# Kernel tuning notes

Measured on AMD Instinct MI355X. Metric: run time of the kernel, lower is better.

Reference implementation:

```python
import jax, jax.numpy as jnp
from jax import lax
import numpy as np


def make_hippo_matrix(N):
    P = np.sqrt(1 + 2 * np.arange(N))
    A = P[:, None] * P[None, :]
    A = np.tril(A) - np.diag(np.arange(N))
    return jnp.asarray(-A, dtype=jnp.float32)


def setup_inputs() -> dict:
    key = jax.random.key(0)
    k1, k2, k3, k4, k5 = jax.random.split(key, 5)
    Bsz, L, H, N = 16, 2048, 512, 64
    dt_min, dt_max = 0.001, 0.1
    u = jax.random.normal(k1, (Bsz, L, H), dtype=jnp.float32)
    B_ssm = jax.random.normal(k2, (N, 1), dtype=jnp.float32)
    C_ssm = jax.random.normal(k3, (1, N), dtype=jnp.float32)
    D_skip = jax.random.normal(k4, (1,), dtype=jnp.float32)
    log_dt = (jax.random.uniform(k5, (1,), dtype=jnp.float32)
              * (np.log(dt_max) - np.log(dt_min)) + np.log(dt_min))
    return {"u": u, "B_ssm": B_ssm, "C_ssm": C_ssm, "D_skip": D_skip, "log_dt": log_dt}


def reference(u, B_ssm, C_ssm, D_skip, log_dt):
    Bsz, L, H = u.shape
    N = B_ssm.shape[0]
    A = make_hippo_matrix(N)  # fixed HiPPO buffer (non-trainable)

    # --- discretize: A_bar = expm(dt*A); B_bar = A^{-1} (A_bar - I) B ---
    dt = jnp.exp(log_dt)  # (1,)
    A_bar = jax.scipy.linalg.expm(dt * A)  # (N, N)
    B_bar = jnp.linalg.solve(A, (A_bar - jnp.eye(N, dtype=A.dtype)) @ B_ssm)  # (N, 1)

    # --- kernel K[k] = C @ A_bar^k @ B_bar, k = 0..L-1, via scan ---
    def step(power, _):
        kk = (C_ssm @ power)[0, 0]
        return A_bar @ power, kk
    _, K = lax.scan(step, B_bar, None, length=L)  # (L,)

    # torch F.conv1d is cross-correlation; with padding L-1 and keeping the
    # first L outputs this equals a causal convolution with the FLIPPED kernel:
    #   y[t] = sum_{m=0}^{t} K[L-1-m] * u[t-m]
    Krev = K[::-1]
    n_fft = 2 * L  # linear (non-circular) convolution
    Uf = jnp.fft.rfft(u, n=n_fft, axis=1)            # (B, n_fft//2+1, H)
    Kf = jnp.fft.rfft(Krev, n=n_fft)                 # (n_fft//2+1,)
    y_conv = jnp.fft.irfft(Uf * Kf[None, :, None], n=n_fft, axis=1)[:, :L, :]
    y = y_conv.astype(u.dtype) + D_skip * u
    return y
```

## Files before the change

kernel.cpp:

```cpp
#include <hip/hip_runtime.h>
#include <math.h>


typedef short short8 __attribute__((ext_vector_type(8)));
typedef short short4v __attribute__((ext_vector_type(4)));
typedef float f32x4 __attribute__((ext_vector_type(4)));

#define SWMASK 28
__device__ __forceinline__ int swz(int r, int c) {
  return (r << 6) + (c ^ (r & SWMASK));
}
__device__ __forceinline__ float Aval(int i, int j) {
  if (i > j)  return -(float)(sqrt(2.0 * i + 1.0) * sqrt(2.0 * j + 1.0));
  if (i == j) return -(float)(i + 1);
  return 0.0f;
}
__device__ __forceinline__ unsigned rne_bf16(float x) {
  unsigned u = __float_as_uint(x);
  return (u + 0x7FFFu + ((u >> 16) & 1u)) >> 16;
}
__device__ __forceinline__ float invfact(int k) {
  switch (k) {
    case 0: return 1.0f;            case 1: return 1.0f;
    case 2: return 0.5f;            case 3: return (float)(1.0/6.0);
    case 4: return (float)(1.0/24.0);       case 5: return (float)(1.0/120.0);
    case 6: return (float)(1.0/720.0);      case 7: return (float)(1.0/5040.0);
    case 8: return (float)(1.0/40320.0);    default: return (float)(1.0/362880.0);
  }
}
__device__ __forceinline__ int slotU(int row, int kg) {
  return (row << 6) + ((kg ^ (row & 7)) << 3);
}
__device__ __forceinline__ float bf2f(unsigned short s) {
  return __uint_as_float(((unsigned)s) << 16);
}
__device__ __forceinline__ unsigned short bfh(float x) {
  return (unsigned short)rne_bf16(x);
}
__device__ __forceinline__ unsigned short bfl(float x, unsigned short h) {
  return (unsigned short)rne_bf16(x - __uint_as_float(((unsigned)h) << 16));
}

__device__ __forceinline__ void mmMFMA(
    const unsigned short* rowLh, const unsigned short* rowLl,
    const unsigned short* colRh, const unsigned short* colRl,
    unsigned short* oColH, unsigned short* oColL,
    unsigned short* oRowH, unsigned short* oRowL,
    float* oF32, const float* Xg, float cI, float cX, int tid) {
  const int lane = tid & 63, w = tid >> 6;
  const int g = lane >> 4, m = lane & 15;
  const bool doN = (oColH != nullptr) || (oF32 != nullptr);
  const bool doT = (oRowH != nullptr);
  f32x4 an[4], at[4];

  if (doN) {
    short8 ah[2], al[2];
#pragma unroll
    for (int kt = 0; kt < 2; ++kt) {
      ah[kt] = *(const short8*)&rowLh[slotU(16 * w + m, 4 * kt + g)];
      al[kt] = *(const short8*)&rowLl[slotU(16 * w + m, 4 * kt + g)];
    }
#pragma unroll
    for (int nt = 0; nt < 4; ++nt) {
      an[nt] = (f32x4){0.f, 0.f, 0.f, 0.f};
#pragma unroll
      for (int kt = 0; kt < 2; ++kt) {
        short8 bh = *(const short8*)&colRh[slotU(16 * nt + m, 4 * kt + g)];
        short8 bl = *(const short8*)&colRl[slotU(16 * nt + m, 4 * kt + g)];
        an[nt] = __builtin_amdgcn_mfma_f32_16x16x32_bf16(ah[kt], bh, an[nt], 0, 0, 0);
        an[nt] = __builtin_amdgcn_mfma_f32_16x16x32_bf16(ah[kt], bl, an[nt], 0, 0, 0);
        an[nt] = __builtin_amdgcn_mfma_f32_16x16x32_bf16(al[kt], bh, an[nt], 0, 0, 0);
      }
      if (Xg) {
#pragma unroll
        for (int r = 0; r < 4; ++r) {
          int rc = 16 * w + 4 * g + r, cc = 16 * nt + m;
          float gv = cX * Xg[(rc << 6) + (cc ^ (rc & 28))];
          if (rc == cc) gv += cI;
          an[nt][r] += gv;
        }
      }
    }
  }
  if (doT) {
    short8 ah[2], al[2];
#pragma unroll
    for (int kt = 0; kt < 2; ++kt) {
      ah[kt] = *(const short8*)&colRh[slotU(16 * w + m, 4 * kt + g)];
      al[kt] = *(const short8*)&colRl[slotU(16 * w + m, 4 * kt + g)];
    }
#pragma unroll
    for (int nt = 0; nt < 4; ++nt) {
      at[nt] = (f32x4){0.f, 0.f, 0.f, 0.f};
#pragma unroll
      for (int kt = 0; kt < 2; ++kt) {
        short8 bh = *(const short8*)&rowLh[slotU(16 * nt + m, 4 * kt + g)];
        short8 bl = *(const short8*)&rowLl[slotU(16 * nt + m, 4 * kt + g)];
        at[nt] = __builtin_amdgcn_mfma_f32_16x16x32_bf16(ah[kt], bh, at[nt], 0, 0, 0);
        at[nt] = __builtin_amdgcn_mfma_f32_16x16x32_bf16(ah[kt], bl, at[nt], 0, 0, 0);
        at[nt] = __builtin_amdgcn_mfma_f32_16x16x32_bf16(al[kt], bh, at[nt], 0, 0, 0);
      }
      if (Xg) {
        int rc = 16 * nt + m;
        int cb = 16 * w + 4 * g;
        f32x4 xv = *(const f32x4*)&Xg[(rc << 6) + (cb ^ (rc & 28))];
#pragma unroll
        for (int r = 0; r < 4; ++r) {
          float gv = cX * xv[r];
          if (rc == cb + r) gv += cI;
          at[nt][r] += gv;
        }
      }
    }
  }
  __syncthreads();
  const int k0 = 16 * w + 4 * g;
  if (doN) {
#pragma unroll
    for (int nt = 0; nt < 4; ++nt) {
      if (oColH) {
        short4v h4, l4;
#pragma unroll
        for (int r = 0; r < 4; ++r) {
          unsigned short h = bfh(an[nt][r]);
          h4[r] = (short)h;
          l4[r] = (short)bfl(an[nt][r], h);
        }
        int s = slotU(16 * nt + m, k0 >> 3) + (k0 & 7);
        *(short4v*)&oColH[s] = h4;
        *(short4v*)&oColL[s] = l4;
      }
      if (oF32) {
#pragma unroll
        for (int r = 0; r < 4; ++r) {
          int rc = k0 + r;
          oF32[(rc << 6) + ((16 * nt + m) ^ (rc & 28))] = an[nt][r];
        }
      }
    }
  }
  if (doT) {
#pragma unroll
    for (int nt = 0; nt < 4; ++nt) {
      short4v h4, l4;
#pragma unroll
      for (int r = 0; r < 4; ++r) {
        unsigned short h = bfh(at[nt][r]);
        h4[r] = (short)h;
        l4[r] = (short)bfl(at[nt][r], h);
      }
      int s = slotU(16 * nt + m, k0 >> 3) + (k0 & 7);
      *(short4v*)&oRowH[s] = h4;
      *(short4v*)&oRowL[s] = l4;
    }
  }
  __syncthreads();
}

__global__ __launch_bounds__(256) void prep_quant(
    const float* __restrict__ u, const float* __restrict__ B_ssm,
    const float* __restrict__ C_ssm, const float* __restrict__ D_skip,
    const float* __restrict__ log_dt, uint4* __restrict__ rg_hi,
    uint4* __restrict__ rg_lo, int* __restrict__ wsi,
    uint4* __restrict__ ubf) {
  __shared__ __align__(16) float smem[16384];
  const int tid = threadIdx.x;

  if (blockIdx.x != 0) {
    int q = blockIdx.x - 1;
    int b = q >> 7, rem = q & 127;
    int tc = rem >> 1, hf = rem & 1;
    int t0 = (tc << 5) + (hf << 4);
    float* S = smem;
#pragma unroll
    for (int r = 0; r < 8; ++r) {
      int s = tid + (r << 8);
      int row = s >> 7, c4 = (s & 127) << 2;
      float4 v = *(const float4*)(u + ((((b << 11) + t0 + row) << 9) + c4));
      *(float4*)&S[row * 520 + c4] = v;
    }
    __syncthreads();
#pragma unroll
    for (int r = 0; r < 4; ++r) {
      int gidx = tid + (r << 8);
      int jnG = gidx >> 5;
      int gl = (gidx >> 4) & 1;
      int hm = gidx & 15;
      int gg = (hf << 1) | gl;
      int h = (jnG << 4) + hm;
      int tb = gl << 3;
      unsigned pk[4];
#pragma unroll
      for (int q2 = 0; q2 < 4; ++q2) {
        unsigned lo = rne_bf16(S[(tb + 2 * q2) * 520 + h]);
        unsigned hi = rne_bf16(S[(tb + 2 * q2 + 1) * 520 + h]);
        pk[q2] = lo | (hi << 16);
      }
      ubf[(((b << 6) | tc) << 11) | (jnG << 6) | (gg << 4) | hm] =
          make_uint4(pk[0], pk[1], pk[2], pk[3]);
    }
    return;
  }

  float* b0 = smem;
  float* b1 = smem + 4096;
  float* b2 = smem + 8192;
  float* b3 = smem + 12288;
  unsigned short* RH = (unsigned short*)b2;
  unsigned short* RL = RH + 4096;
  unsigned short* CH = (unsigned short*)b3;
  unsigned short* CL = CH + 4096;
  unsigned short* X2H = (unsigned short*)b1;
  unsigned short* X2L = X2H + 4096;
  double* Pd = (double*)b3;
  const int lane = tid & 63, wv = tid >> 6;
  const float dtf = expf(log_dt[0]);

  if (tid < 64) {
    double p = sqrt(2.0 * tid + 1.0);
    Pd[tid] = p;
    double s = p;
#pragma unroll
    for (int off = 1; off < 64; off <<= 1) {
      double t = __shfl_down(s, off, 64);
      if (tid + off < 64) s += t;
    }
    b2[tid] = (float)((tid + 1.0) + p * (s - p));
  }
  __syncthreads();
  float maxc = 0.f;
  for (int j = 0; j < 64; ++j) maxc = fmaxf(maxc, b2[j]);
  int iE;
  frexpf(dtf * maxc, &iE);
  int sExp = iE > 0 ? iE : 0;
  const float scale = ldexpf(dtf, -sExp);
  __syncthreads();

  const int r0i = (tid & 15) << 2, c0i = (tid >> 4) << 2;
  double pr_[4], pc_[4];
#pragma unroll
  for (int i = 0; i < 4; ++i) pr_[i] = Pd[r0i + i];
#pragma unroll
  for (int j = 0; j < 4; ++j) pc_[j] = Pd[c0i + j];
  __syncthreads();
  float xv[4][4];
  unsigned short xh[4][4], xl[4][4];
#pragma unroll
  for (int i = 0; i < 4; ++i)
#pragma unroll
    for (int j = 0; j < 4; ++j) {
      int ri = r0i + i, cj = c0i + j;
      float a;
      if (ri > cj)       a = -(float)(pr_[i] * pc_[j]);
      else if (ri == cj) a = -(float)(ri + 1);
      else               a = 0.0f;
      float x = scale * a;
      xv[i][j] = x;
      xh[i][j] = bfh(x);
      xl[i][j] = bfl(x, xh[i][j]);
      b0[swz(ri, cj)] = x;
    }
#pragma unroll
  for (int i = 0; i < 4; ++i) {
    short4v h4, l4;
#pragma unroll
    for (int j = 0; j < 4; ++j) { h4[j] = (short)xh[i][j]; l4[j] = (short)xl[i][j]; }
    int s = slotU(r0i + i, c0i >> 3) + (c0i & 7);
    *(short4v*)&RH[s] = h4;
    *(short4v*)&RL[s] = l4;
  }
#pragma unroll
  for (int j = 0; j < 4; ++j) {
    short4v h4, l4;
#pragma unroll
    for (int i = 0; i < 4; ++i) { h4[i] = (short)xh[i][j]; l4[i] = (short)xl[i][j]; }
    int s = slotU(c0i + j, r0i >> 3) + (r0i & 7);
    *(short4v*)&CH[s] = h4;
    *(short4v*)&CL[s] = l4;
  }
  __syncthreads();

  mmMFMA(RH, RL, CH, CL, X2H, X2L, nullptr, nullptr, nullptr, nullptr,
         0.f, 0.f, tid);

#pragma unroll
  for (int i = 0; i < 4; ++i) {
    short4v h4, l4;
#pragma unroll
    for (int j = 0; j < 4; ++j) {
      float gv = invfact(9) * xv[i][j];
      if (r0i + i == c0i + j) gv += invfact(8);
      unsigned short h = bfh(gv);
      h4[j] = (short)h;
      l4[j] = (short)bfl(gv, h);
    }
    int s = slotU(r0i + i, c0i >> 3) + (c0i & 7);
    *(short4v*)&RH[s] = h4;
    *(short4v*)&RL[s] = l4;
  }
  __syncthreads();

  for (int mq = 3; mq >= 1; --mq)
    mmMFMA(RH, RL, X2H, X2L, nullptr, nullptr, RH, RL, nullptr, b0,
           invfact(2 * mq), invfact(2 * mq + 1), tid);
  mmMFMA(RH, RL, X2H, X2L, CH, CL, RH, RL, b1, b0, 0.f, 1.f, tid);

  for (int q = 0; q < sExp; ++q)
    mmMFMA(RH, RL, CH, CL, CH, CL, RH, RL, b1, b1, 0.f, 2.f, tid);

  float* Bl = b0 + 64;
  if (tid < 64) {
    Bl[tid] = B_ssm[tid];
    int d = tid;
    float x = b1[(d << 6) + (d ^ (d & 28))] + 1.0f;
    unsigned short h = bfh(x), l = bfl(x, h);
    int s = slotU(d, d >> 3) + (d & 7);
    RH[s] = h; RL[s] = l; CH[s] = h; CL[s] = l;
  }
  __syncthreads();

  if (tid < 64) {
    int i = tid;
    double pi = sqrt(2.0 * i + 1.0);
    double accd = 0.0;
#pragma unroll
    for (int k4 = 0; k4 < 16; ++k4) {
      int jM = (k4 << 2) ^ (i & 28);
      float4 mv = *(const float4*)&b1[(i << 6) + jM];
      float4 bv = *(const float4*)&Bl[k4 << 2];
      accd += (double)mv.x * bv.x + (double)mv.y * bv.y +
              (double)mv.z * bv.z + (double)mv.w * bv.w;
    }
    double xvv = 0.0;
    for (int j = 0; j < 64; ++j) {
      if (i == j) xvv = accd / (-(double)(j + 1));
      double xj = __shfl(xvv, j, 64);
      double pj = __shfl(pi, j, 64);
      if (i > j) accd += pi * pj * xj;
    }
    b0[i] = (float)xvv;
    b1[(i << 6) + (i ^ (i & 28))] += 1.0f;
  }
  __syncthreads();

  for (int k = 0; k < 6; ++k) {
    int cnt = 1 << k;
    for (int t = wv; t < cnt; t += 4) {
      float a0 = 0.f, a1 = 0.f;
#pragma unroll
      for (int k4 = 0; k4 < 16; ++k4) {
        int jM = (k4 << 2) ^ (lane & 28);
        f32x4 mv = *(const f32x4*)&b1[(lane << 6) + jM];
        f32x4 vvv = *(const f32x4*)&b0[(t << 6) + ((k4 << 2) ^ (t & 28))];
        a0 = fmaf(mv[0], vvv[0], fmaf(mv[1], vvv[1], a0));
        a1 = fmaf(mv[2], vvv[2], fmaf(mv[3], vvv[3], a1));
      }
      int td = t + cnt;
      b0[(td << 6) + (lane ^ (td & 28))] = a0 + a1;
    }
    mmMFMA(RH, RL, CH, CL, CH, CL, RH, RL, b1, nullptr, 0.f, 0.f, tid);
  }

  if (tid < 64) b1[tid] = C_ssm[tid];
  __syncthreads();
  for (int k = 0; k < 5; ++k) {
    int cnt = 1 << k;
    for (int t = wv; t < cnt; t += 4) {
      float ah = 0.f, al = 0.f;
#pragma unroll
      for (int kg = 0; kg < 8; ++kg) {
        short8 ch8 = *(const short8*)&CH[slotU(lane, kg)];
        short8 cl8 = *(const short8*)&CL[slotU(lane, kg)];
        f32x4 w0 = *(const f32x4*)&b1[(t << 6) + (kg << 3)];
        f32x4 w1 = *(const f32x4*)&b1[(t << 6) + (kg << 3) + 4];
#pragma unroll
        for (int j = 0; j < 4; ++j) {
          ah = fmaf(bf2f((unsigned short)ch8[j]), w0[j], ah);
          al = fmaf(bf2f((unsigned short)cl8[j]), w0[j], al);
        }
#pragma unroll
        for (int j = 0; j < 4; ++j) {
          ah = fmaf(bf2f((unsigned short)ch8[4 + j]), w1[j], ah);
          al = fmaf(bf2f((unsigned short)cl8[4 + j]), w1[j], al);
        }
      }
      b1[((t + cnt) << 6) + lane] = ah + al;
    }
    if (k < 3) {
      mmMFMA(RH, RL, CH, CL, CH, CL, RH, RL, nullptr, nullptr, 0.f, 0.f, tid);
    } else if (k == 3) {
      mmMFMA(RH, RL, CH, CL, CH, CL, nullptr, nullptr, nullptr, nullptr,
             0.f, 0.f, tid);
    } else {
      __syncthreads();
    }
  }

  float* K = b3;
  for (int x = tid; x < 2048; x += 256) {
    int tp = x >> 6, t = x & 63;
    float d0 = 0.f, d1 = 0.f;
#pragma unroll
    for (int i4 = 0; i4 < 64; i4 += 4) {
      f32x4 wv4 = *(const f32x4*)&b1[(tp << 6) + i4];
      f32x4 vv4 = *(const f32x4*)&b0[(t << 6) + (i4 ^ (t & 28))];
      d0 = fmaf(wv4[0], vv4[0], fmaf(wv4[1], vv4[1], d0));
      d1 = fmaf(wv4[2], vv4[2], fmaf(wv4[3], vv4[3], d1));
    }
    K[x] = d0 + d1;
  }
  __syncthreads();

  unsigned short* kh = (unsigned short*)b2;
  unsigned short* kl = kh + 2192;
  float* ss = (float*)(kh + 4400);
  const float D = D_skip[0];
  for (int x = tid; x < 2192; x += 256) {
    float v = 0.f;
    if (x < 2048) { v = K[x]; if (x == 2047) v += D; }
    unsigned h = rne_bf16(v);
    float hf2 = __uint_as_float(h << 16);
    unsigned l = rne_bf16(v - hf2);
    kh[x] = (unsigned short)h;
    kl[x] = (unsigned short)l;
  }
  {
    float ssum = 0.f;
#pragma unroll
    for (int q = 0; q < 8; ++q) {
      int x = (tid << 3) + q;
      float v = K[x];
      if (x == 2047) v += D;
      ssum += v * v;
    }
    ss[tid] = ssum;
  }
  __syncthreads();

  for (int e = tid; e < 2176; e += 256) {
    unsigned ph[4], pl[4];
#pragma unroll
    for (int q2 = 0; q2 < 4; ++q2) {
      ph[q2] = (unsigned)kh[e + 2 * q2] | ((unsigned)kh[e + 2 * q2 + 1] << 16);
      pl[q2] = (unsigned)kl[e + 2 * q2] | ((unsigned)kl[e + 2 * q2 + 1] << 16);
    }
    rg_hi[e] = make_uint4(ph[0], ph[1], ph[2], ph[3]);
    rg_lo[e] = make_uint4(pl[0], pl[1], pl[2], pl[3]);
  }
  if (tid == 0) {
    float accq = 0.f;
    int xt = 0;
    for (int jc = 255; jc >= 0; --jc) {
      float na = accq + ss[jc];
      if (na > 4e-8f) { xt = (jc + 1) << 3; break; }
      accq = na;
    }
    wsi[0] = 2048 - xt;
  }
}

__device__ __forceinline__ void load_bfrag(short8* bf, const uint4* ubf,
                                           const float* u, int use_ubf, int b,
                                           int kt, int h0, int wn, int lane) {
  if (use_ubf) {
    const short8* base = (const short8*)(ubf + ((((b << 6) | kt) << 11) |
                                               (((h0 >> 4) + (wn << 2)) << 6) |
                                               lane));
#pragma unroll
    for (int j = 0; j < 4; ++j) bf[j] = base[j << 6];
  } else {
    int gg = lane >> 4, hm = lane & 15;
#pragma unroll
    for (int j = 0; j < 4; ++j) {
      const float* src = u + ((((b << 11) + (kt << 5) + (gg << 3)) << 9) + h0 +
                              (((wn << 2) + j) << 4) + hm);
      unsigned pk[4];
#pragma unroll
      for (int q = 0; q < 4; ++q) {
        unsigned lo = rne_bf16(src[q << 10]);
        unsigned hi = rne_bf16(src[(q << 10) + 512]);
        pk[q] = lo | (hi << 16);
      }
      uint4 vv = make_uint4(pk[0], pk[1], pk[2], pk[3]);
      bf[j] = __builtin_bit_cast(short8, vv);
    }
  }
}

__global__ __launch_bounds__(256) void conv_kernel(
    const float* __restrict__ u, const uint4* __restrict__ rg_hi,
    const uint4* __restrict__ rg_lo, const uint4* __restrict__ ubf,
    const int* __restrict__ wsi, float* __restrict__ y, int use_ubf) {
  __shared__ __align__(16) unsigned ringh[1024], ringl[1024];
  const int tid = threadIdx.x;
  const int bid0 = blockIdx.x;
  const int bid = ((bid0 & 7) << 6) | (bid0 >> 3);
  const int b = bid >> 5;
  const int bn = bid & 3;
  const int pr = (bid >> 2) & 7;
  const int h0 = bn << 7;
  const int lane = tid & 63, w = tid >> 6;
  const int wm = w & 1, wn = w >> 1;
  const int g = lane >> 4, m = lane & 15;
  const int D_lo = wsi[0];

  for (int tile = 0; tile < 2; ++tile) {
    const int bm = tile ? pr : 15 - pr;
    const int l0 = bm << 7;
    const int e0 = 1920 - l0;
    const int ktiles = 4 * bm + 4;
    int kt_lim = ((l0 + 127 - D_lo) >> 5) + 1;
    if (kt_lim < 0) kt_lim = 0;
    if (kt_lim > ktiles) kt_lim = ktiles;

    __syncthreads();
    for (int tsk = tid; tsk < 432; tsk += 256) {
      int isLo = tsk >= 216;
      int e = e0 + (isLo ? tsk - 216 : tsk);
      if (e <= 2175) {
        uint4 v = isLo ? rg_lo[e] : rg_hi[e];
        ((uint4*)(isLo ? ringl : ringh))[e & 255] = v;
      }
    }

    f32x4 acc[4][4];
#pragma unroll
    for (int i = 0; i < 4; ++i)
#pragma unroll
      for (int j = 0; j < 4; ++j) acc[i][j] = (f32x4){0.f, 0.f, 0.f, 0.f};

    short8 bcur[4];
    if (kt_lim > 0) load_bfrag(bcur, ubf, u, use_ubf, b, 0, h0, wn, lane);

    for (int kt = 0; kt < kt_lim; ++kt) {
      __syncthreads();
      uint4 tv;
      bool tdo = false;
      int tslot = 0;
      const bool tlo = (tid >= 32);
      if (tid < 64) {
        int te = e0 + 216 + (kt << 5) + (tid & 31);
        if (te <= 2175) {
          tv = tlo ? rg_lo[te] : rg_hi[te];
          tdo = true;
          tslot = te & 255;
        }
      }
      const int ebase = 2047 - l0 + (kt << 5) - (wm << 6) - m + (g << 3);
      short8 ah[4], al[4];
#pragma unroll
      for (int i = 0; i < 4; ++i) {
        int slot = (ebase - (i << 4)) & 255;
        ah[i] = ((const short8*)ringh)[slot];
        al[i] = ((const short8*)ringl)[slot];
      }
      short8 bnx[4];
      if (kt + 1 < kt_lim)
        load_bfrag(bnx, ubf, u, use_ubf, b, kt + 1, h0, wn, lane);
#pragma unroll
      for (int i = 0; i < 4; ++i)
#pragma unroll
        for (int j = 0; j < 4; ++j) {
          acc[i][j] = __builtin_amdgcn_mfma_f32_16x16x32_bf16(ah[i], bcur[j],
                                                              acc[i][j], 0, 0, 0);
          acc[i][j] = __builtin_amdgcn_mfma_f32_16x16x32_bf16(al[i], bcur[j],
                                                              acc[i][j], 0, 0, 0);
        }
      if (tdo) ((uint4*)(tlo ? ringl : ringh))[tslot] = tv;
      if (kt + 1 < kt_lim) {
#pragma unroll
        for (int j = 0; j < 4; ++j) bcur[j] = bnx[j];
      }
    }

#pragma unroll
    for (int i = 0; i < 4; ++i)
#pragma unroll
      for (int j = 0; j < 4; ++j) {
        int l = l0 + (wm << 6) + (i << 4) + (g << 2);
        int h = h0 + (((wn << 2) + j) << 4) + m;
        int off = (((b << 11) + l) << 9) + h;
#pragma unroll
        for (int r = 0; r < 4; ++r) y[off + (r << 9)] = acc[i][j][r];
      }
  }
}

extern "C" void kernel_launch(void* const* d_in, const int* in_sizes, int n_in,
                              void* d_out, int out_size, void* d_ws,
                              size_t ws_size, hipStream_t stream) {
  (void)in_sizes; (void)n_in; (void)out_size;
  const float* u = (const float*)d_in[0];
  const float* B_ssm = (const float*)d_in[1];
  const float* C_ssm = (const float*)d_in[2];
  const float* D_skip = (const float*)d_in[3];
  const float* log_dt = (const float*)d_in[4];
  float* y = (float*)d_out;

  const size_t UBF_BYTES = (size_t)16 * 64 * 2048 * 16;
  const size_t RG_BYTES = (size_t)2176 * 16 * 2 + 256;
  int use_ubf = (ws_size >= UBF_BYTES + RG_BYTES) ? 1 : 0;
  char* wsb = (char*)d_ws;
  uint4* ubf = (uint4*)wsb;
  uint4* rg_hi = use_ubf ? (uint4*)(wsb + UBF_BYTES) : (uint4*)wsb;
  uint4* rg_lo = rg_hi + 2176;
  int* wsi = (int*)(rg_lo + 2176);

  prep_quant<<<use_ubf ? 2049 : 1, 256, 0, stream>>>(
      u, B_ssm, C_ssm, D_skip, log_dt, rg_hi, rg_lo, wsi, ubf);
  conv_kernel<<<512, 256, 0, stream>>>(u, rg_hi, rg_lo, ubf, wsi, y, use_ubf);
}
```

Before: 211.5 us.

## Widen prep kernel to 1024 threads and split MFMA tiles across 16 waves

The prep_quant kernel now launches with 1024 threads instead of 256. The 64x64 matrix products in mmMFMA are spread so each of 16 waves computes one 16x16 output tile rather than four. The u-quantization blocks and the K-kernel loops are restrided to match the larger block. The goal is to shorten the serial single-block expm/power chain, at the cost of more barrier participants and possibly lower occupancy for the 2048 quantization blocks.

```diff
diff --git a/kernel.cpp b/kernel.cpp
--- a/kernel.cpp
+++ b/kernel.cpp
@@ -9,11 +9,6 @@
 #define SWMASK 28
 __device__ __forceinline__ int swz(int r, int c) {
   return (r << 6) + (c ^ (r & SWMASK));
-}
-__device__ __forceinline__ float Aval(int i, int j) {
-  if (i > j)  return -(float)(sqrt(2.0 * i + 1.0) * sqrt(2.0 * j + 1.0));
-  if (i == j) return -(float)(i + 1);
-  return 0.0f;
 }
 __device__ __forceinline__ unsigned rne_bf16(float x) {
   unsigned u = __float_as_uint(x);
@@ -48,116 +43,96 @@
     unsigned short* oRowH, unsigned short* oRowL,
     float* oF32, const float* Xg, float cI, float cX, int tid) {
   const int lane = tid & 63, w = tid >> 6;
+  const int wr = w & 3, wc = w >> 2;
   const int g = lane >> 4, m = lane & 15;
   const bool doN = (oColH != nullptr) || (oF32 != nullptr);
   const bool doT = (oRowH != nullptr);
-  f32x4 an[4], at[4];
+  f32x4 an = (f32x4){0.f, 0.f, 0.f, 0.f};
+  f32x4 at = (f32x4){0.f, 0.f, 0.f, 0.f};
 
   if (doN) {
-    short8 ah[2], al[2];
 #pragma unroll
     for (int kt = 0; kt < 2; ++kt) {
-      ah[kt] = *(const short8*)&rowLh[slotU(16 * w + m, 4 * kt + g)];
-      al[kt] = *(const short8*)&rowLl[slotU(16 * w + m, 4 * kt + g)];
-    }
-#pragma unroll
-    for (int nt = 0; nt < 4; ++nt) {
-      an[nt] = (f32x4){0.f, 0.f, 0.f, 0.f};
-#pragma unroll
-      for (int kt = 0; kt < 2; ++kt) {
-        short8 bh = *(const short8*)&colRh[slotU(16 * nt + m, 4 * kt + g)];
-        short8 bl = *(const short8*)&colRl[slotU(16 * nt + m, 4 * kt + g)];
-        an[nt] = __builtin_amdgcn_mfma_f32_16x16x32_bf16(ah[kt], bh, an[nt], 0, 0, 0);
-        an[nt] = __builtin_amdgcn_mfma_f32_16x16x32_bf16(ah[kt], bl, an[nt], 0, 0, 0);
-        an[nt] = __builtin_amdgcn_mfma_f32_16x16x32_bf16(al[kt], bh, an[nt], 0, 0, 0);
-      }
-      if (Xg) {
-#pragma unroll
-        for (int r = 0; r < 4; ++r) {
-          int rc = 16 * w + 4 * g + r, cc = 16 * nt + m;
-          float gv = cX * Xg[(rc << 6) + (cc ^ (rc & 28))];
-          if (rc == cc) gv += cI;
-          an[nt][r] += gv;
-        }
+      short8 ah = *(const short8*)&rowLh[slotU(16 * wr + m, 4 * kt + g)];
+      short8 al = *(const short8*)&rowLl[slotU(16 * wr + m, 4 * kt + g)];
+      short8 bh = *(const short8*)&colRh[slotU(16 * wc + m, 4 * kt + g)];
+      short8 bl = *(const short8*)&colRl[slotU(16 * wc + m, 4 * kt + g)];
+      an = __builtin_amdgcn_mfma_f32_16x16x32_bf16(ah, bh, an, 0, 0, 0);
+      an = __builtin_amdgcn_mfma_f32_16x16x32_bf16(ah, bl, an, 0, 0, 0);
+      an = __builtin_amdgcn_mfma_f32_16x16x32_bf16(al, bh, an, 0, 0, 0);
+    }
+    if (Xg) {
+#pragma unroll
+      for (int r = 0; r < 4; ++r) {
+        int rc = 16 * wr + 4 * g + r, cc = 16 * wc + m;
+        float gv = cX * Xg[(rc << 6) + (cc ^ (rc & 28))];
+        if (rc == cc) gv += cI;
+        an[r] += gv;
       }
     }
   }
   if (doT) {
-    short8 ah[2], al[2];
 #pragma unroll
     for (int kt = 0; kt < 2; ++kt) {
-      ah[kt] = *(const short8*)&colRh[slotU(16 * w + m, 4 * kt + g)];
-      al[kt] = *(const short8*)&colRl[slotU(16 * w + m, 4 * kt + g)];
-    }
-#pragma unroll
-    for (int nt = 0; nt < 4; ++nt) {
-      at[nt] = (f32x4){0.f, 0.f, 0.f, 0.f};
-#pragma unroll
-      for (int kt = 0; kt < 2; ++kt) {
-        short8 bh = *(const short8*)&rowLh[slotU(16 * nt + m, 4 * kt + g)];
-        short8 bl = *(const short8*)&rowLl[slotU(16 * nt + m, 4 * kt + g)];
-        at[nt] = __builtin_amdgcn_mfma_f32_16x16x32_bf16(ah[kt], bh, at[nt], 0, 0, 0);
-        at[nt] = __builtin_amdgcn_mfma_f32_16x16x32_bf16(ah[kt], bl, at[nt], 0, 0, 0);
-        at[nt] = __builtin_amdgcn_mfma_f32_16x16x32_bf16(al[kt], bh, at[nt], 0, 0, 0);
-      }
-      if (Xg) {
-        int rc = 16 * nt + m;
-        int cb = 16 * w + 4 * g;
-        f32x4 xv = *(const f32x4*)&Xg[(rc << 6) + (cb ^ (rc & 28))];
-#pragma unroll
-        for (int r = 0; r < 4; ++r) {
-          float gv = cX * xv[r];
-          if (rc == cb + r) gv += cI;
-          at[nt][r] += gv;
-        }
-      }
-    }
-  }
-  __syncthreads();
-  const int k0 = 16 * w + 4 * g;
+      short8 ah = *(const short8*)&colRh[slotU(16 * wr + m, 4 * kt + g)];
+      short8 al = *(const short8*)&colRl[slotU(16 * wr + m, 4 * kt + g)];
+      short8 bh = *(const short8*)&rowLh[slotU(16 * wc + m, 4 * kt + g)];
+      short8 bl = *(const short8*)&rowLl[slotU(16 * wc + m, 4 * kt + g)];
+      at = __builtin_amdgcn_mfma_f32_16x16x32_bf16(ah, bh, at, 0, 0, 0);
+      at = __builtin_amdgcn_mfma_f32_16x16x32_bf16(ah, bl, at, 0, 0, 0);
+      at = __builtin_amdgcn_mfma_f32_16x16x32_bf16(al, bh, at, 0, 0, 0);
+    }
+    if (Xg) {
+      int rc = 16 * wc + m;
+      int cb = 16 * wr + 4 * g;
+      f32x4 xv = *(const f32x4*)&Xg[(rc << 6) + (cb ^ (rc & 28))];
+#pragma unroll
+      for (int r = 0; r < 4; ++r) {
+        float gv = cX * xv[r];
+        if (rc == cb + r) gv += cI;
+        at[r] += gv;
+      }
+    }
+  }
+  __syncthreads();
+  const int k0 = 16 * wr + 4 * g;
   if (doN) {
-#pragma unroll
-    for (int nt = 0; nt < 4; ++nt) {
-      if (oColH) {
-        short4v h4, l4;
-#pragma unroll
-        for (int r = 0; r < 4; ++r) {
-          unsigned short h = bfh(an[nt][r]);
-          h4[r] = (short)h;
-          l4[r] = (short)bfl(an[nt][r], h);
-        }
-        int s = slotU(16 * nt + m, k0 >> 3) + (k0 & 7);
-        *(short4v*)&oColH[s] = h4;
-        *(short4v*)&oColL[s] = l4;
-      }
-      if (oF32) {
-#pragma unroll
-        for (int r = 0; r < 4; ++r) {
-          int rc = k0 + r;
-          oF32[(rc << 6) + ((16 * nt + m) ^ (rc & 28))] = an[nt][r];
-        }
+    if (oColH) {
+      short4v h4, l4;
+#pragma unroll
+      for (int r = 0; r < 4; ++r) {
+        unsigned short h = bfh(an[r]);
+        h4[r] = (short)h;
+        l4[r] = (short)bfl(an[r], h);
+      }
+      int s = slotU(16 * wc + m, k0 >> 3) + (k0 & 7);
+      *(short4v*)&oColH[s] = h4;
+      *(short4v*)&oColL[s] = l4;
+    }
+    if (oF32) {
+#pragma unroll
+      for (int r = 0; r < 4; ++r) {
+        int rc = k0 + r;
+        oF32[(rc << 6) + ((16 * wc + m) ^ (rc & 28))] = an[r];
       }
     }
   }
   if (doT) {
-#pragma unroll
-    for (int nt = 0; nt < 4; ++nt) {
-      short4v h4, l4;
-#pragma unroll
-      for (int r = 0; r < 4; ++r) {
-        unsigned short h = bfh(at[nt][r]);
-        h4[r] = (short)h;
-        l4[r] = (short)bfl(at[nt][r], h);
-      }
-      int s = slotU(16 * nt + m, k0 >> 3) + (k0 & 7);
-      *(short4v*)&oRowH[s] = h4;
-      *(short4v*)&oRowL[s] = l4;
-    }
-  }
-  __syncthreads();
-}
-
-__global__ __launch_bounds__(256) void prep_quant(
+    short4v h4, l4;
+#pragma unroll
+    for (int r = 0; r < 4; ++r) {
+      unsigned short h = bfh(at[r]);
+      h4[r] = (short)h;
+      l4[r] = (short)bfl(at[r], h);
+    }
+    int s = slotU(16 * wc + m, k0 >> 3) + (k0 & 7);
+    *(short4v*)&oRowH[s] = h4;
+    *(short4v*)&oRowL[s] = l4;
+  }
+  __syncthreads();
+}
+
+__global__ __launch_bounds__(1024, 1) void prep_quant(
     const float* __restrict__ u, const float* __restrict__ B_ssm,
     const float* __restrict__ C_ssm, const float* __restrict__ D_skip,
     const float* __restrict__ log_dt, uint4* __restrict__ rg_hi,
@@ -173,16 +148,15 @@
     int t0 = (tc << 5) + (hf << 4);
     float* S = smem;
 #pragma unroll
-    for (int r = 0; r < 8; ++r) {
-      int s = tid + (r << 8);
+    for (int r = 0; r < 2; ++r) {
+      int s = tid + (r << 10);
       int row = s >> 7, c4 = (s & 127) << 2;
       float4 v = *(const float4*)(u + ((((b << 11) + t0 + row) << 9) + c4));
       *(float4*)&S[row * 520 + c4] = v;
     }
     __syncthreads();
-#pragma unroll
-    for (int r = 0; r < 4; ++r) {
-      int gidx = tid + (r << 8);
+    {
+      int gidx = tid;
       int jnG = gidx >> 5;
       int gl = (gidx >> 4) & 1;
       int hm = gidx & 15;
@@ -236,67 +210,73 @@
   const float scale = ldexpf(dtf, -sExp);
   __syncthreads();
 
-  const int r0i = (tid & 15) << 2, c0i = (tid >> 4) << 2;
+  const int r0i = (tid & 15) << 2, c0i = ((tid >> 4) & 15) << 2;
   double pr_[4], pc_[4];
-#pragma unroll
-  for (int i = 0; i < 4; ++i) pr_[i] = Pd[r0i + i];
-#pragma unroll
-  for (int j = 0; j < 4; ++j) pc_[j] = Pd[c0i + j];
-  __syncthreads();
   float xv[4][4];
-  unsigned short xh[4][4], xl[4][4];
-#pragma unroll
-  for (int i = 0; i < 4; ++i)
+  if (tid < 256) {
+#pragma unroll
+    for (int i = 0; i < 4; ++i) pr_[i] = Pd[r0i + i];
+#pragma unroll
+    for (int j = 0; j < 4; ++j) pc_[j] = Pd[c0i + j];
+  }
+  __syncthreads();
+  if (tid < 256) {
+    unsigned short xh[4][4], xl[4][4];
+#pragma unroll
+    for (int i = 0; i < 4; ++i)
+#pragma unroll
+      for (int j = 0; j < 4; ++j) {
+        int ri = r0i + i, cj = c0i + j;
+        float a;
+        if (ri > cj)       a = -(float)(pr_[i] * pc_[j]);
+        else if (ri == cj) a = -(float)(ri + 1);
+        else               a = 0.0f;
+        float x = scale * a;
+        xv[i][j] = x;
+        xh[i][j] = bfh(x);
+        xl[i][j] = bfl(x, xh[i][j]);
+        b0[swz(ri, cj)] = x;
+      }
+#pragma unroll
+    for (int i = 0; i < 4; ++i) {
+      short4v h4, l4;
+#pragma unroll
+      for (int j = 0; j < 4; ++j) { h4[j] = (short)xh[i][j]; l4[j] = (short)xl[i][j]; }
+      int s = slotU(r0i + i, c0i >> 3) + (c0i & 7);
+      *(short4v*)&RH[s] = h4;
+      *(short4v*)&RL[s] = l4;
+    }
 #pragma unroll
     for (int j = 0; j < 4; ++j) {
-      int ri = r0i + i, cj = c0i + j;
-      float a;
-      if (ri > cj)       a = -(float)(pr_[i] * pc_[j]);
-      else if (ri == cj) a = -(float)(ri + 1);
-      else               a = 0.0f;
-      float x = scale * a;
-      xv[i][j] = x;
-      xh[i][j] = bfh(x);
-      xl[i][j] = bfl(x, xh[i][j]);
-      b0[swz(ri, cj)] = x;
-    }
-#pragma unroll
-  for (int i = 0; i < 4; ++i) {
-    short4v h4, l4;
-#pragma unroll
-    for (int j = 0; j < 4; ++j) { h4[j] = (short)xh[i][j]; l4[j] = (short)xl[i][j]; }
-    int s = slotU(r0i + i, c0i >> 3) + (c0i & 7);
-    *(short4v*)&RH[s] = h4;
-    *(short4v*)&RL[s] = l4;
-  }
-#pragma unroll
-  for (int j = 0; j < 4; ++j) {
-    short4v h4, l4;
-#pragma unroll
-    for (int i = 0; i < 4; ++i) { h4[i] = (short)xh[i][j]; l4[i] = (short)xl[i][j]; }
-    int s = slotU(c0i + j, r0i >> 3) + (r0i & 7);
-    *(short4v*)&CH[s] = h4;
-    *(short4v*)&CL[s] = l4;
+      short4v h4, l4;
+#pragma unroll
+      for (int i = 0; i < 4; ++i) { h4[i] = (short)xh[i][j]; l4[i] = (short)xl[i][j]; }
+      int s = slotU(c0i + j, r0i >> 3) + (r0i & 7);
+      *(short4v*)&CH[s] = h4;
+      *(short4v*)&CL[s] = l4;
+    }
   }
   __syncthreads();
 
   mmMFMA(RH, RL, CH, CL, X2H, X2L, nullptr, nullptr, nullptr, nullptr,
          0.f, 0.f, tid);
 
-#pragma unroll
-  for (int i = 0; i < 4; ++i) {
-    short4v h4, l4;
-#pragma unroll
-    for (int j = 0; j < 4; ++j) {
-      float gv = invfact(9) * xv[i][j];
-      if (r0i + i == c0i + j) gv += invfact(8);
-      unsigned short h = bfh(gv);
-      h4[j] = (short)h;
-      l4[j] = (short)bfl(gv, h);
-    }
-    int s = slotU(r0i + i, c0i >> 3) + (c0i & 7);
-    *(short4v*)&RH[s] = h4;
-    *(short4v*)&RL[s] = l4;
+  if (tid < 256) {
+#pragma unroll
+    for (int i = 0; i < 4; ++i) {
+      short4v h4, l4;
+#pragma unroll
+      for (int j = 0; j < 4; ++j) {
+        float gv = invfact(9) * xv[i][j];
+        if (r0i + i == c0i + j) gv += invfact(8);
+        unsigned short h = bfh(gv);
+        h4[j] = (short)h;
+        l4[j] = (short)bfl(gv, h);
+      }
+      int s = slotU(r0i + i, c0i >> 3) + (c0i & 7);
+      *(short4v*)&RH[s] = h4;
+      *(short4v*)&RL[s] = l4;
+    }
   }
   __syncthreads();
 
@@ -345,7 +325,7 @@
 
   for (int k = 0; k < 6; ++k) {
     int cnt = 1 << k;
-    for (int t = wv; t < cnt; t += 4) {
+    for (int t = wv; t < cnt; t += 16) {
       float a0 = 0.f, a1 = 0.f;
 #pragma unroll
       for (int k4 = 0; k4 < 16; ++k4) {
@@ -365,7 +345,7 @@
   __syncthreads();
   for (int k = 0; k < 5; ++k) {
     int cnt = 1 << k;
-    for (int t = wv; t < cnt; t += 4) {
+    for (int t = wv; t < cnt; t += 16) {
       float ah = 0.f, al = 0.f;
 #pragma unroll
       for (int kg = 0; kg < 8; ++kg) {
@@ -397,7 +377,7 @@
   }
 
   float* K = b3;
-  for (int x = tid; x < 2048; x += 256) {
+  for (int x = tid; x < 2048; x += 1024) {
     int tp = x >> 6, t = x & 63;
     float d0 = 0.f, d1 = 0.f;
 #pragma unroll
@@ -415,7 +395,7 @@
   unsigned short* kl = kh + 2192;
   float* ss = (float*)(kh + 4400);
   const float D = D_skip[0];
-  for (int x = tid; x < 2192; x += 256) {
+  for (int x = tid; x < 2192; x += 1024) {
     float v = 0.f;
     if (x < 2048) { v = K[x]; if (x == 2047) v += D; }
     unsigned h = rne_bf16(v);
@@ -424,7 +404,7 @@
     kh[x] = (unsigned short)h;
     kl[x] = (unsigned short)l;
   }
-  {
+  if (tid < 256) {
     float ssum = 0.f;
 #pragma unroll
     for (int q = 0; q < 8; ++q) {
@@ -437,7 +417,7 @@
   }
   __syncthreads();
 
-  for (int e = tid; e < 2176; e += 256) {
+  for (int e = tid; e < 2176; e += 1024) {
     unsigned ph[4], pl[4];
 #pragma unroll
     for (int q2 = 0; q2 < 4; ++q2) {
@@ -606,7 +586,7 @@
   uint4* rg_lo = rg_hi + 2176;
   int* wsi = (int*)(rg_lo + 2176);
 
-  prep_quant<<<use_ubf ? 2049 : 1, 256, 0, stream>>>(
+  prep_quant<<<use_ubf ? 2049 : 1, 1024, 0, stream>>>(
       u, B_ssm, C_ssm, D_skip, log_dt, rg_hi, rg_lo, wsi, ubf);
   conv_kernel<<<512, 256, 0, stream>>>(u, rg_hi, rg_lo, ubf, wsi, y, use_ubf);
 }
```

Result: faster. 202.5 us (-4.2%).
